# Kernel optimization log

Measured on AMD Instinct MI355X. Metric: run time of the kernel, lower is better.

Reference implementation:

```python
import jax, jax.numpy as jnp
import numpy as np

B, S, D = 32, 2048, 64
SQRT_DIM = float(np.sqrt(D))  # scale=True -> divide by sqrt(dim)


def setup_inputs() -> dict:
    key = jax.random.key(0)
    kq, kk, kv, km = jax.random.split(key, 4)
    query = jax.random.normal(kq, (B, S, D), dtype=jnp.float32)
    key_t = jax.random.normal(kk, (B, S, D), dtype=jnp.float32)
    value = jax.random.normal(kv, (B, S, D), dtype=jnp.float32)
    mask = jax.random.randint(km, (B, S, S), 0, 2).astype(jnp.bool_)
    return {"query": query, "key": key_t, "value": value, "mask": mask}


def reference(query, key, value, mask):
    # score = Q @ K^T / sqrt(dim)   -> [B, S, S]
    score = jnp.einsum('bqd,bkd->bqk', query, key) / SQRT_DIM
    score = jnp.where(mask, jnp.float32(-1e9), score)  # masked_fill_
    attn = jax.nn.softmax(score, axis=-1)
    # context = attn @ V   -> [B, S, D]  (block_mask is None -> no gamma)
    context = jnp.einsum('bqk,bkd->bqd', attn, value)
    return (context, attn)
```

## Files before the change

### kernel.cpp

```cpp
#include <hip/hip_runtime.h>
#include <hip/hip_bf16.h>

#define BB 32
#define SS 2048
#define DD 64
#define NTH 256
#define QT 16
#define KTL 128
#define SCALE 0.125f

typedef __attribute__((ext_vector_type(4))) float f32x4;
typedef __attribute__((ext_vector_type(8))) short bf16x8;

union B8 { bf16x8 v; unsigned int u[4]; };

__device__ __forceinline__ unsigned int pk2bf(float a, float b) {
    __hip_bfloat162 h = __float22bfloat162_rn(make_float2(a, b));
    unsigned int u;
    __builtin_memcpy(&u, &h, 4);
    return u;
}
__device__ __forceinline__ float bf_lo(unsigned int w) {
    return __builtin_bit_cast(float, w << 16);
}
__device__ __forceinline__ float bf_hi(unsigned int w) {
    return __builtin_bit_cast(float, w & 0xffff0000u);
}

__global__ __launch_bounds__(NTH) void prepK(const float* __restrict__ K,
                                             unsigned short* __restrict__ Kbf) {
    const size_t i = (size_t)blockIdx.x * NTH + threadIdx.x;
    const float4* s = (const float4*)K;
    const float4 a = s[2 * i], c = s[2 * i + 1];
    uint4 w;
    w.x = pk2bf(a.x, a.y); w.y = pk2bf(a.z, a.w);
    w.z = pk2bf(c.x, c.y); w.w = pk2bf(c.z, c.w);
    ((uint4*)Kbf)[i] = w;
}

#define VPADF 68
__global__ __launch_bounds__(NTH) void prepV(const float* __restrict__ V,
                                             unsigned short* __restrict__ VTh,
                                             unsigned short* __restrict__ VTl) {
    __shared__ __align__(16) float lt[KTL * VPADF];
    const int t  = threadIdx.x;
    const int b  = blockIdx.x >> 4;
    const int ck = blockIdx.x & 15;
    const float4* Vs = (const float4*)(V + ((size_t)b * SS + ck * KTL) * DD);
    #pragma unroll
    for (int i = 0; i < 8; ++i) {
        const int f4 = i * NTH + t;
        float4 v = Vs[f4];
        const int kc = f4 >> 4, d4 = f4 & 15;
        *(float4*)&lt[kc * VPADF + d4 * 4] = v;
    }
    __syncthreads();
    const int d = t >> 2, kseg = t & 3;
    unsigned short* oh = VTh + ((size_t)b * DD + d) * SS + ck * KTL + kseg * 32;
    unsigned short* ol = VTl + ((size_t)b * DD + d) * SS + ck * KTL + kseg * 32;
    #pragma unroll
    for (int cch = 0; cch < 4; ++cch) {
        uint4 wh, wl;
        unsigned int* ph = (unsigned int*)&wh;
        unsigned int* pl = (unsigned int*)&wl;
        #pragma unroll
        for (int p = 0; p < 4; ++p) {
            const int k0 = kseg * 32 + cch * 8 + p * 2;
            const float a = lt[k0 * VPADF + d], c = lt[(k0 + 1) * VPADF + d];
            const unsigned int hw = pk2bf(a, c);
            ph[p] = hw;
            pl[p] = pk2bf(a - bf_lo(hw), c - bf_hi(hw));
        }
        *(uint4*)(oh + cch * 8) = wh;
        *(uint4*)(ol + cch * 8) = wl;
    }
}

__global__ __launch_bounds__(NTH) void packM(const int* __restrict__ M,
                                             unsigned int* __restrict__ Mp) {
    const int t = threadIdx.x, w = t >> 6, l = t & 63;
    const size_t row = (size_t)blockIdx.x * 4 + w;
    const int* mr = M + row * SS;
    const int kb = (l >> 4) * 32 + (l & 15);
    unsigned int bits = 0;
    #pragma unroll
    for (int tl = 0; tl < 16; ++tl) {
        const int m0 = __builtin_nontemporal_load(&mr[tl * 128 + kb]);
        const int m1 = __builtin_nontemporal_load(&mr[tl * 128 + kb + 16]);
        bits |= (m0 ? 1u : 0u) << (2 * tl);
        bits |= (m1 ? 1u : 0u) << (2 * tl + 1);
    }
    Mp[row * 64 + l] = bits;
}

__global__ __launch_bounds__(NTH, 8) void sdpa_mfma2(
    const float* __restrict__ Q, const unsigned int* __restrict__ Mp,
    const unsigned short* __restrict__ Kbf,
    const unsigned short* __restrict__ VTh, const unsigned short* __restrict__ VTl,
    float* __restrict__ ctx, float* __restrict__ attn)
{
    __shared__ __align__(16) unsigned char smem[17408];
    __shared__ float wsum[4][QT];
    __shared__ float inv_l[QT];
    unsigned short* bnc = (unsigned short*)smem;
    float*          scr = (float*)smem;

    const int t    = threadIdx.x;
    const int wave = t >> 6, l = t & 63, g = l >> 4, li = l & 15;
    const unsigned int bid = blockIdx.x;
    const unsigned int swz = (bid & 7) * 512 + (bid >> 3);
    const int b    = swz >> 7;
    const int q0   = (swz & 127) * QT;

    const unsigned short* Kb  = Kbf + (size_t)b * SS * DD;
    const unsigned short* Vhb = VTh + (size_t)b * DD * SS;
    const unsigned short* Vlb = VTl + (size_t)b * DD * SS;
    float* attb = attn + ((size_t)b * SS + q0) * SS;

    unsigned int mreg[4];
    {
        const unsigned int* Mpb = Mp + ((size_t)b * SS + q0) * 64 + (wave * 16 + li);
        #pragma unroll
        for (int r = 0; r < 4; ++r) mreg[r] = Mpb[(size_t)(g * 4 + r) * 64];
    }

    B8 qh[2], ql[2];
    {
        const float* qp = Q + ((size_t)(b * SS + q0 + li)) * DD + g * 8;
        #pragma unroll
        for (int h = 0; h < 2; ++h) {
            float f[8];
            *(float4*)&f[0] = *(const float4*)(qp + h * 32);
            *(float4*)&f[4] = *(const float4*)(qp + h * 32 + 4);
            #pragma unroll
            for (int i = 0; i < 4; ++i) {
                unsigned int hw = pk2bf(f[2*i], f[2*i+1]);
                qh[h].u[i] = hw;
                ql[h].u[i] = pk2bf(f[2*i] - bf_lo(hw), f[2*i+1] - bf_hi(hw));
            }
        }
    }

    const unsigned short* kf0 = Kb + (size_t)(wave * 32 + li) * DD + g * 8;

    auto qk = [&](int tl, f32x4& s0, f32x4& s1) {
        const unsigned short* p0 = kf0 + (size_t)tl * KTL * DD;
        #pragma unroll
        for (int h = 0; h < 2; ++h) {
            B8 k0, k1;
            k0.v = *(const bf16x8*)(p0 + 32 * h);
            k1.v = *(const bf16x8*)(p0 + 16 * DD + 32 * h);
            s0 = __builtin_amdgcn_mfma_f32_16x16x32_bf16(qh[h].v, k0.v, s0, 0, 0, 0);
            s0 = __builtin_amdgcn_mfma_f32_16x16x32_bf16(ql[h].v, k0.v, s0, 0, 0, 0);
            s1 = __builtin_amdgcn_mfma_f32_16x16x32_bf16(qh[h].v, k1.v, s1, 0, 0, 0);
            s1 = __builtin_amdgcn_mfma_f32_16x16x32_bf16(ql[h].v, k1.v, s1, 0, 0, 0);
        }
    };

    float lsum[4] = {0.f, 0.f, 0.f, 0.f};

    #pragma unroll 1
    for (int tl = 0; tl < 16; ++tl) {
        f32x4 s0 = {0.f,0.f,0.f,0.f}, s1 = {0.f,0.f,0.f,0.f};
        qk(tl, s0, s1);
        #pragma unroll
        for (int r = 0; r < 4; ++r) {
            const float e0 = ((mreg[r] >> (2 * tl))     & 1u) ? 0.f : __expf(s0[r] * SCALE);
            const float e1 = ((mreg[r] >> (2 * tl + 1)) & 1u) ? 0.f : __expf(s1[r] * SCALE);
            lsum[r] += e0 + e1;
        }
    }

    #pragma unroll
    for (int off = 8; off >= 1; off >>= 1)
        #pragma unroll
        for (int r = 0; r < 4; ++r)
            lsum[r] += __shfl_xor(lsum[r], off, 64);
    if (li == 0) {
        #pragma unroll
        for (int r = 0; r < 4; ++r) wsum[wave][g * 4 + r] = lsum[r];
    }
    __syncthreads();
    if (t < QT) inv_l[t] = 1.0f / (wsum[0][t] + wsum[1][t] + wsum[2][t] + wsum[3][t]);
    __syncthreads();
    float invl[4];
    #pragma unroll
    for (int r = 0; r < 4; ++r) invl[r] = inv_l[g * 4 + r];

    f32x4 cacc[4] = {{0.f,0.f,0.f,0.f},{0.f,0.f,0.f,0.f},{0.f,0.f,0.f,0.f},{0.f,0.f,0.f,0.f}};
    unsigned short* bw = bnc + wave * 512;

    #pragma unroll 1
    for (int tl = 0; tl < 16; ++tl) {
        f32x4 s0 = {0.f,0.f,0.f,0.f}, s1 = {0.f,0.f,0.f,0.f};
        qk(tl, s0, s1);
        const int kg0 = tl * KTL + wave * 32 + li;
        #pragma unroll
        for (int r = 0; r < 4; ++r) {
            const float e0 = ((mreg[r] >> (2 * tl))     & 1u) ? 0.f : __expf(s0[r] * SCALE);
            const float e1 = ((mreg[r] >> (2 * tl + 1)) & 1u) ? 0.f : __expf(s1[r] * SCALE);
            const size_t ao = (size_t)(g * 4 + r) * SS + kg0;
            attb[ao]      = e0 * invl[r];
            attb[ao + 16] = e1 * invl[r];
            const int q = g * 4 + r;
            const int b0 = li >> 3, b1 = (li + 16) >> 3;
            bw[((b0 * 16 + (q ^ b0)) << 3) + (li & 7)] = (unsigned short)pk2bf(e0, 0.f);
            bw[((b1 * 16 + (q ^ b1)) << 3) + (li & 7)] = (unsigned short)pk2bf(e1, 0.f);
        }
        B8 pf;
        pf.v = *(const bf16x8*)(bw + ((g * 16 + (li ^ g)) << 3));
        const size_t vcol = (size_t)tl * KTL + wave * 32 + g * 8;
        #pragma unroll
        for (int c = 0; c < 4; ++c) {
            const size_t voff = (size_t)(c * 16 + li) * SS + vcol;
            B8 vh, vl;
            vh.v = *(const bf16x8*)(Vhb + voff);
            vl.v = *(const bf16x8*)(Vlb + voff);
            cacc[c] = __builtin_amdgcn_mfma_f32_16x16x32_bf16(pf.v, vh.v, cacc[c], 0, 0, 0);
            cacc[c] = __builtin_amdgcn_mfma_f32_16x16x32_bf16(pf.v, vl.v, cacc[c], 0, 0, 0);
        }
    }

    __syncthreads();
    {
        const int row = wave * 64 + l;
        #pragma unroll
        for (int c = 0; c < 4; ++c)
            #pragma unroll
            for (int r = 0; r < 4; ++r)
                scr[row * 17 + c * 4 + r] = cacc[c][r];
    }
    __syncthreads();
    {
        const int q = t >> 4, d0 = (t & 15) * 4;
        float4 o;
        float* op = &o.x;
        #pragma unroll
        for (int dd = 0; dd < 4; ++dd) {
            const int d    = d0 + dd;
            const int lane = (q >> 2) * 16 + (d & 15);
            const int idx  = lane * 17 + (d >> 4) * 4 + (q & 3);
            float s = 0.f;
            #pragma unroll
            for (int w = 0; w < 4; ++w) s += scr[w * 64 * 17 + idx];
            op[dd] = s * inv_l[q];
        }
        *(float4*)(ctx + ((size_t)(b * SS + q0 + q)) * DD + d0) = o;
    }
}

extern "C" void kernel_launch(void* const* d_in, const int* in_sizes, int n_in,
                              void* d_out, int out_size, void* d_ws, size_t ws_size,
                              hipStream_t stream) {
    const float* Q = (const float*)d_in[0];
    const float* K = (const float*)d_in[1];
    const float* V = (const float*)d_in[2];
    const int*   M = (const int*)d_in[3];
    float* ctx  = (float*)d_out;
    float* attn = (float*)d_out + (size_t)BB * SS * DD;

    const size_t NE = (size_t)BB * SS * DD;
    unsigned short* Kbf = (unsigned short*)d_ws;
    unsigned short* VTh = Kbf + NE;
    unsigned short* VTl = VTh + NE;
    unsigned int*   Mpk = (unsigned int*)(VTl + NE);

    prepK<<<dim3((unsigned)(NE / 8 / NTH)), dim3(NTH), 0, stream>>>(K, Kbf);
    prepV<<<dim3(BB * (SS / KTL)), dim3(NTH), 0, stream>>>(V, VTh, VTl);
    packM<<<dim3(BB * SS / 4), dim3(NTH), 0, stream>>>(M, Mpk);
    sdpa_mfma2<<<dim3(BB * (SS / QT)), dim3(NTH), 0, stream>>>(Q, Mpk, Kbf, VTh, VTl, ctx, attn);
}
```

Before: 1.386 ms.

## Process two 16-row query tiles per block and write attn as float2 pairs

Each block now handles 32 query rows as two MFMA M-tiles, so every K and V fragment loaded from global memory feeds twice as many MFMAs. Key columns are remapped so each lane owns two adjacent columns; attn stores become 8-byte float2 writes and probabilities are packed as bf16 pairs into LDS, with the mask bit-packing updated to match. The cost is more registers per thread, so the occupancy hint drops from 8 to 3 blocks, and the grid is halved, which may hurt latency hiding.

```diff
diff --git a/kernel.cpp b/kernel.cpp
--- a/kernel.cpp
+++ b/kernel.cpp
@@ -5,7 +5,7 @@
 #define SS 2048
 #define DD 64
 #define NTH 256
-#define QT 16
+#define QT 32
 #define KTL 128
 #define SCALE 0.125f
 
@@ -81,19 +81,19 @@
     const int t = threadIdx.x, w = t >> 6, l = t & 63;
     const size_t row = (size_t)blockIdx.x * 4 + w;
     const int* mr = M + row * SS;
-    const int kb = (l >> 4) * 32 + (l & 15);
+    const int kb = (l >> 4) * 32 + 2 * (l & 15);
     unsigned int bits = 0;
     #pragma unroll
     for (int tl = 0; tl < 16; ++tl) {
         const int m0 = __builtin_nontemporal_load(&mr[tl * 128 + kb]);
-        const int m1 = __builtin_nontemporal_load(&mr[tl * 128 + kb + 16]);
+        const int m1 = __builtin_nontemporal_load(&mr[tl * 128 + kb + 1]);
         bits |= (m0 ? 1u : 0u) << (2 * tl);
         bits |= (m1 ? 1u : 0u) << (2 * tl + 1);
     }
     Mp[row * 64 + l] = bits;
 }
 
-__global__ __launch_bounds__(NTH, 8) void sdpa_mfma2(
+__global__ __launch_bounds__(NTH, 3) void sdpa_mfma3(
     const float* __restrict__ Q, const unsigned int* __restrict__ Mp,
     const unsigned short* __restrict__ Kbf,
     const unsigned short* __restrict__ VTh, const unsigned short* __restrict__ VTl,
@@ -108,25 +108,29 @@
     const int t    = threadIdx.x;
     const int wave = t >> 6, l = t & 63, g = l >> 4, li = l & 15;
     const unsigned int bid = blockIdx.x;
-    const unsigned int swz = (bid & 7) * 512 + (bid >> 3);
-    const int b    = swz >> 7;
-    const int q0   = (swz & 127) * QT;
+    const unsigned int swz = (bid & 7) * 256 + (bid >> 3);
+    const int b    = swz >> 6;
+    const int q0   = (swz & 63) * QT;
 
     const unsigned short* Kb  = Kbf + (size_t)b * SS * DD;
     const unsigned short* Vhb = VTh + (size_t)b * DD * SS;
     const unsigned short* Vlb = VTl + (size_t)b * DD * SS;
     float* attb = attn + ((size_t)b * SS + q0) * SS;
 
-    unsigned int mreg[4];
+    unsigned int mreg[2][4];
     {
         const unsigned int* Mpb = Mp + ((size_t)b * SS + q0) * 64 + (wave * 16 + li);
         #pragma unroll
-        for (int r = 0; r < 4; ++r) mreg[r] = Mpb[(size_t)(g * 4 + r) * 64];
-    }
-
-    B8 qh[2], ql[2];
-    {
-        const float* qp = Q + ((size_t)(b * SS + q0 + li)) * DD + g * 8;
+        for (int mt = 0; mt < 2; ++mt)
+            #pragma unroll
+            for (int r = 0; r < 4; ++r)
+                mreg[mt][r] = Mpb[(size_t)(mt * 16 + g * 4 + r) * 64];
+    }
+
+    B8 qh[2][2], ql[2][2];
+    #pragma unroll
+    for (int mt = 0; mt < 2; ++mt) {
+        const float* qp = Q + ((size_t)(b * SS + q0 + mt * 16 + li)) * DD + g * 8;
         #pragma unroll
         for (int h = 0; h < 2; ++h) {
             float f[8];
@@ -135,80 +139,97 @@
             #pragma unroll
             for (int i = 0; i < 4; ++i) {
                 unsigned int hw = pk2bf(f[2*i], f[2*i+1]);
-                qh[h].u[i] = hw;
-                ql[h].u[i] = pk2bf(f[2*i] - bf_lo(hw), f[2*i+1] - bf_hi(hw));
-            }
-        }
-    }
-
-    const unsigned short* kf0 = Kb + (size_t)(wave * 32 + li) * DD + g * 8;
-
-    auto qk = [&](int tl, f32x4& s0, f32x4& s1) {
-        const unsigned short* p0 = kf0 + (size_t)tl * KTL * DD;
+                qh[mt][h].u[i] = hw;
+                ql[mt][h].u[i] = pk2bf(f[2*i] - bf_lo(hw), f[2*i+1] - bf_hi(hw));
+            }
+        }
+    }
+
+    const unsigned short* kfE = Kb + (size_t)(wave * 32 + 2 * li) * DD + g * 8;
+
+    auto qk = [&](int tl, f32x4 sE[2], f32x4 sO[2]) {
+        const unsigned short* p0 = kfE + (size_t)tl * KTL * DD;
         #pragma unroll
         for (int h = 0; h < 2; ++h) {
-            B8 k0, k1;
-            k0.v = *(const bf16x8*)(p0 + 32 * h);
-            k1.v = *(const bf16x8*)(p0 + 16 * DD + 32 * h);
-            s0 = __builtin_amdgcn_mfma_f32_16x16x32_bf16(qh[h].v, k0.v, s0, 0, 0, 0);
-            s0 = __builtin_amdgcn_mfma_f32_16x16x32_bf16(ql[h].v, k0.v, s0, 0, 0, 0);
-            s1 = __builtin_amdgcn_mfma_f32_16x16x32_bf16(qh[h].v, k1.v, s1, 0, 0, 0);
-            s1 = __builtin_amdgcn_mfma_f32_16x16x32_bf16(ql[h].v, k1.v, s1, 0, 0, 0);
+            B8 kE, kO;
+            kE.v = *(const bf16x8*)(p0 + 32 * h);
+            kO.v = *(const bf16x8*)(p0 + DD + 32 * h);
+            #pragma unroll
+            for (int mt = 0; mt < 2; ++mt) {
+                sE[mt] = __builtin_amdgcn_mfma_f32_16x16x32_bf16(qh[mt][h].v, kE.v, sE[mt], 0, 0, 0);
+                sE[mt] = __builtin_amdgcn_mfma_f32_16x16x32_bf16(ql[mt][h].v, kE.v, sE[mt], 0, 0, 0);
+                sO[mt] = __builtin_amdgcn_mfma_f32_16x16x32_bf16(qh[mt][h].v, kO.v, sO[mt], 0, 0, 0);
+                sO[mt] = __builtin_amdgcn_mfma_f32_16x16x32_bf16(ql[mt][h].v, kO.v, sO[mt], 0, 0, 0);
+            }
         }
     };
 
-    float lsum[4] = {0.f, 0.f, 0.f, 0.f};
+    float lsum[2][4] = {{0.f,0.f,0.f,0.f},{0.f,0.f,0.f,0.f}};
 
     #pragma unroll 1
     for (int tl = 0; tl < 16; ++tl) {
-        f32x4 s0 = {0.f,0.f,0.f,0.f}, s1 = {0.f,0.f,0.f,0.f};
-        qk(tl, s0, s1);
-        #pragma unroll
-        for (int r = 0; r < 4; ++r) {
-            const float e0 = ((mreg[r] >> (2 * tl))     & 1u) ? 0.f : __expf(s0[r] * SCALE);
-            const float e1 = ((mreg[r] >> (2 * tl + 1)) & 1u) ? 0.f : __expf(s1[r] * SCALE);
-            lsum[r] += e0 + e1;
-        }
+        f32x4 sE[2] = {{0.f,0.f,0.f,0.f},{0.f,0.f,0.f,0.f}};
+        f32x4 sO[2] = {{0.f,0.f,0.f,0.f},{0.f,0.f,0.f,0.f}};
+        qk(tl, sE, sO);
+        #pragma unroll
+        for (int mt = 0; mt < 2; ++mt)
+            #pragma unroll
+            for (int r = 0; r < 4; ++r) {
+                const float eE = ((mreg[mt][r] >> (2 * tl))     & 1u) ? 0.f : __expf(sE[mt][r] * SCALE);
+                const float eO = ((mreg[mt][r] >> (2 * tl + 1)) & 1u) ? 0.f : __expf(sO[mt][r] * SCALE);
+                lsum[mt][r] += eE + eO;
+            }
     }
 
     #pragma unroll
     for (int off = 8; off >= 1; off >>= 1)
         #pragma unroll
-        for (int r = 0; r < 4; ++r)
-            lsum[r] += __shfl_xor(lsum[r], off, 64);
+        for (int mt = 0; mt < 2; ++mt)
+            #pragma unroll
+            for (int r = 0; r < 4; ++r)
+                lsum[mt][r] += __shfl_xor(lsum[mt][r], off, 64);
     if (li == 0) {
         #pragma unroll
-        for (int r = 0; r < 4; ++r) wsum[wave][g * 4 + r] = lsum[r];
+        for (int mt = 0; mt < 2; ++mt)
+            #pragma unroll
+            for (int r = 0; r < 4; ++r) wsum[wave][mt * 16 + g * 4 + r] = lsum[mt][r];
     }
     __syncthreads();
     if (t < QT) inv_l[t] = 1.0f / (wsum[0][t] + wsum[1][t] + wsum[2][t] + wsum[3][t]);
     __syncthreads();
-    float invl[4];
-    #pragma unroll
-    for (int r = 0; r < 4; ++r) invl[r] = inv_l[g * 4 + r];
-
-    f32x4 cacc[4] = {{0.f,0.f,0.f,0.f},{0.f,0.f,0.f,0.f},{0.f,0.f,0.f,0.f},{0.f,0.f,0.f,0.f}};
-    unsigned short* bw = bnc + wave * 512;
+    float invl[2][4];
+    #pragma unroll
+    for (int mt = 0; mt < 2; ++mt)
+        #pragma unroll
+        for (int r = 0; r < 4; ++r) invl[mt][r] = inv_l[mt * 16 + g * 4 + r];
+
+    f32x4 cacc[2][4] = {{{0.f,0.f,0.f,0.f},{0.f,0.f,0.f,0.f},{0.f,0.f,0.f,0.f},{0.f,0.f,0.f,0.f}},
+                        {{0.f,0.f,0.f,0.f},{0.f,0.f,0.f,0.f},{0.f,0.f,0.f,0.f},{0.f,0.f,0.f,0.f}}};
+    unsigned short* bw = bnc + wave * 1024;
 
     #pragma unroll 1
     for (int tl = 0; tl < 16; ++tl) {
-        f32x4 s0 = {0.f,0.f,0.f,0.f}, s1 = {0.f,0.f,0.f,0.f};
-        qk(tl, s0, s1);
-        const int kg0 = tl * KTL + wave * 32 + li;
-        #pragma unroll
-        for (int r = 0; r < 4; ++r) {
-            const float e0 = ((mreg[r] >> (2 * tl))     & 1u) ? 0.f : __expf(s0[r] * SCALE);
-            const float e1 = ((mreg[r] >> (2 * tl + 1)) & 1u) ? 0.f : __expf(s1[r] * SCALE);
-            const size_t ao = (size_t)(g * 4 + r) * SS + kg0;
-            attb[ao]      = e0 * invl[r];
-            attb[ao + 16] = e1 * invl[r];
-            const int q = g * 4 + r;
-            const int b0 = li >> 3, b1 = (li + 16) >> 3;
-            bw[((b0 * 16 + (q ^ b0)) << 3) + (li & 7)] = (unsigned short)pk2bf(e0, 0.f);
-            bw[((b1 * 16 + (q ^ b1)) << 3) + (li & 7)] = (unsigned short)pk2bf(e1, 0.f);
-        }
-        B8 pf;
-        pf.v = *(const bf16x8*)(bw + ((g * 16 + (li ^ g)) << 3));
+        f32x4 sE[2] = {{0.f,0.f,0.f,0.f},{0.f,0.f,0.f,0.f}};
+        f32x4 sO[2] = {{0.f,0.f,0.f,0.f},{0.f,0.f,0.f,0.f}};
+        qk(tl, sE, sO);
+        const int kg0 = tl * KTL + wave * 32 + 2 * li;
+        #pragma unroll
+        for (int mt = 0; mt < 2; ++mt) {
+            unsigned short* bwm = bw + mt * 512;
+            #pragma unroll
+            for (int r = 0; r < 4; ++r) {
+                const float eE = ((mreg[mt][r] >> (2 * tl))     & 1u) ? 0.f : __expf(sE[mt][r] * SCALE);
+                const float eO = ((mreg[mt][r] >> (2 * tl + 1)) & 1u) ? 0.f : __expf(sO[mt][r] * SCALE);
+                const size_t ao = (size_t)(mt * 16 + g * 4 + r) * SS + kg0;
+                *(float2*)&attb[ao] = make_float2(eE * invl[mt][r], eO * invl[mt][r]);
+                const int q = g * 4 + r;
+                const int blk = li >> 2;
+                *(unsigned int*)&bwm[((blk * 16 + (q ^ blk)) << 3) + 2 * (li & 3)] = pk2bf(eE, eO);
+            }
+        }
+        B8 pf0, pf1;
+        pf0.v = *(const bf16x8*)(bw + ((g * 16 + (li ^ g)) << 3));
+        pf1.v = *(const bf16x8*)(bw + 512 + ((g * 16 + (li ^ g)) << 3));
         const size_t vcol = (size_t)tl * KTL + wave * 32 + g * 8;
         #pragma unroll
         for (int c = 0; c < 4; ++c) {
@@ -216,36 +237,41 @@
             B8 vh, vl;
             vh.v = *(const bf16x8*)(Vhb + voff);
             vl.v = *(const bf16x8*)(Vlb + voff);
-            cacc[c] = __builtin_amdgcn_mfma_f32_16x16x32_bf16(pf.v, vh.v, cacc[c], 0, 0, 0);
-            cacc[c] = __builtin_amdgcn_mfma_f32_16x16x32_bf16(pf.v, vl.v, cacc[c], 0, 0, 0);
-        }
-    }
-
-    __syncthreads();
-    {
-        const int row = wave * 64 + l;
-        #pragma unroll
-        for (int c = 0; c < 4; ++c)
-            #pragma unroll
-            for (int r = 0; r < 4; ++r)
-                scr[row * 17 + c * 4 + r] = cacc[c][r];
-    }
-    __syncthreads();
-    {
-        const int q = t >> 4, d0 = (t & 15) * 4;
-        float4 o;
-        float* op = &o.x;
-        #pragma unroll
-        for (int dd = 0; dd < 4; ++dd) {
-            const int d    = d0 + dd;
-            const int lane = (q >> 2) * 16 + (d & 15);
-            const int idx  = lane * 17 + (d >> 4) * 4 + (q & 3);
-            float s = 0.f;
-            #pragma unroll
-            for (int w = 0; w < 4; ++w) s += scr[w * 64 * 17 + idx];
-            op[dd] = s * inv_l[q];
-        }
-        *(float4*)(ctx + ((size_t)(b * SS + q0 + q)) * DD + d0) = o;
+            cacc[0][c] = __builtin_amdgcn_mfma_f32_16x16x32_bf16(pf0.v, vh.v, cacc[0][c], 0, 0, 0);
+            cacc[0][c] = __builtin_amdgcn_mfma_f32_16x16x32_bf16(pf0.v, vl.v, cacc[0][c], 0, 0, 0);
+            cacc[1][c] = __builtin_amdgcn_mfma_f32_16x16x32_bf16(pf1.v, vh.v, cacc[1][c], 0, 0, 0);
+            cacc[1][c] = __builtin_amdgcn_mfma_f32_16x16x32_bf16(pf1.v, vl.v, cacc[1][c], 0, 0, 0);
+        }
+    }
+
+    #pragma unroll 1
+    for (int mt = 0; mt < 2; ++mt) {
+        __syncthreads();
+        {
+            const int row = wave * 64 + l;
+            #pragma unroll
+            for (int c = 0; c < 4; ++c)
+                #pragma unroll
+                for (int r = 0; r < 4; ++r)
+                    scr[row * 17 + c * 4 + r] = cacc[mt][c][r];
+        }
+        __syncthreads();
+        {
+            const int q = t >> 4, d0 = (t & 15) * 4;
+            float4 o;
+            float* op = &o.x;
+            #pragma unroll
+            for (int dd = 0; dd < 4; ++dd) {
+                const int d    = d0 + dd;
+                const int lane = (q >> 2) * 16 + (d & 15);
+                const int idx  = lane * 17 + (d >> 4) * 4 + (q & 3);
+                float s = 0.f;
+                #pragma unroll
+                for (int w = 0; w < 4; ++w) s += scr[w * 64 * 17 + idx];
+                op[dd] = s * inv_l[mt * 16 + q];
+            }
+            *(float4*)(ctx + ((size_t)(b * SS + q0 + mt * 16 + q)) * DD + d0) = o;
+        }
     }
 }
 
@@ -268,5 +294,5 @@
     prepK<<<dim3((unsigned)(NE / 8 / NTH)), dim3(NTH), 0, stream>>>(K, Kbf);
     prepV<<<dim3(BB * (SS / KTL)), dim3(NTH), 0, stream>>>(V, VTh, VTl);
     packM<<<dim3(BB * SS / 4), dim3(NTH), 0, stream>>>(M, Mpk);
-    sdpa_mfma2<<<dim3(BB * (SS / QT)), dim3(NTH), 0, stream>>>(Q, Mpk, Kbf, VTh, VTl, ctx, attn);
-}
+    sdpa_mfma3<<<dim3(BB * (SS / QT)), dim3(NTH), 0, stream>>>(Q, Mpk, Kbf, VTh, VTl, ctx, attn);
+}
```

Result: faster. 1.200 ms (-13.4%).
